# Performance work log

Measured on AMD Instinct MI355X. Metric: run time of the kernel, lower is better.

Reference implementation:

```python
import jax, jax.numpy as jnp
import numpy as np

POS_THRESHOLD = 0.5
B, N, A = 8, 262144, 64


def setup_inputs() -> dict:
    key = jax.random.key(0)
    k1, k2, k3 = jax.random.split(key, 3)
    # anchors: (y_center, x_center, h, w); centers in [0,1), positive h,w
    anchorss = jax.random.uniform(k1, (B, N, 4), dtype=jnp.float32)
    anchorss = anchorss.at[..., 2:].set(anchorss[..., 2:] * 0.3 + 0.01)  # h,w in (0.01, 0.31)
    # gt boxes as (y1, x1, y2, x2) with y1<y2, x1<x2
    raw = jax.random.uniform(k2, (B, A, 2, 2), dtype=jnp.float32)  # [...,coord_pair,(lo,hi)]
    lo = jnp.min(raw, axis=-1)  # (B,A,2) -> y1,x1
    hi = jnp.max(raw, axis=-1)  # (B,A,2) -> y2,x2
    gt_bboxess = jnp.concatenate([lo, hi], axis=-1)  # (B,A,4) = (y1,x1,y2,x2)
    gt_counts = jax.random.randint(k3, (B, 1), 1, A, dtype=jnp.int32)
    return {"anchorss": anchorss, "gt_bboxess": gt_bboxess,
            "gt_counts": gt_counts, "use_anchor": 1}


def reference(anchorss, gt_bboxess, gt_counts, use_anchor):
    # anchorss: (B,N,4), gt_bboxess: (B,A,4), gt_counts: (B,1)
    if use_anchor:
        y, x, h, w = (anchorss[..., i] for i in range(4))  # (B,N)
        y1 = y - h / 2
        y2 = y1 + h
        x1 = x - w / 2
        x2 = x1 + w
        area = h * w
    else:
        y1, x1, y2, x2 = (anchorss[..., i] for i in range(4))
        area = (y2 - y1) * (x2 - x1)
    gy1, gx1, gy2, gx2 = (gt_bboxess[..., i] for i in range(4))  # (B,A)
    ga = (gy2 - gy1) * (gx2 - gx1)  # (B,A)
    # broadcast anchors (B,N,1) against gts (B,1,A): same clamp math as torch
    yy1 = jnp.clip(y1[:, :, None], gy1[:, None, :], gy2[:, None, :])
    xx1 = jnp.clip(x1[:, :, None], gx1[:, None, :], gx2[:, None, :])
    yy2 = jnp.clip(y2[:, :, None], gy1[:, None, :], gy2[:, None, :])
    xx2 = jnp.clip(x2[:, :, None], gx1[:, None, :], gx2[:, None, :])
    inter = (yy2 - yy1) * (xx2 - xx1)  # (B,N,A)
    union = area[:, :, None] + ga[:, None, :] - inter
    iou = inter / union
    # mask out invalid gts (index >= gt_count per batch)
    valid = jnp.arange(A, dtype=gt_counts.dtype)[None, :] < gt_counts  # (B,A)
    pos = (iou >= POS_THRESHOLD) & valid[:, None, :]  # (B,N,A)
    labels = jnp.any(pos, axis=2).astype(jnp.int32)[..., None]  # (B,N,1)
    return labels
```

## Files before the change

kernel.cpp:

```cpp
#include <hip/hip_runtime.h>

constexpr int BLOCK = 256;
constexpr int IPT = 4;

__global__ __launch_bounds__(BLOCK) void assign_cls_label_kernel(
    const float* __restrict__ anchorss,
    const float* __restrict__ gt_bboxess,
    const int* __restrict__ gt_counts,
    const int* __restrict__ use_anchor_p,
    int* __restrict__ out,
    int N, int A)
{
#pragma clang fp contract(off)
    extern __shared__ float smem[];
    float4* s_box = reinterpret_cast<float4*>(smem);
    float*  s_ga  = smem + 4 * A;
    __shared__ int s_count;

    const int b   = blockIdx.y;
    const int tid = threadIdx.x;

    for (int i = tid; i < A; i += BLOCK) {
        float4 g = reinterpret_cast<const float4*>(gt_bboxess)[(size_t)b * A + i];
        s_box[i] = g;
        s_ga[i]  = (g.z - g.x) * (g.w - g.y);
    }
    if (tid == 0) s_count = gt_counts[b];
    __syncthreads();

    const int count      = s_count;
    const int use_anchor = use_anchor_p[0];

    const int n0 = (blockIdx.x * BLOCK + tid) * IPT;
    if (n0 >= N) return;
    const int nk = min(IPT, N - n0);

    float y1[IPT], x1[IPT], y2[IPT], x2[IPT], area[IPT];
    const float4* arow = reinterpret_cast<const float4*>(anchorss) + (size_t)b * N;
    for (int k = 0; k < IPT; ++k) {
        const int n = (k < nk) ? (n0 + k) : (N - 1);
        float4 a = arow[n];
        if (use_anchor) {
            const float h = a.z, w = a.w;
            y1[k]   = a.x - h * 0.5f;
            y2[k]   = y1[k] + h;
            x1[k]   = a.y - w * 0.5f;
            x2[k]   = x1[k] + w;
            area[k] = h * w;
        } else {
            y1[k] = a.x; x1[k] = a.y; y2[k] = a.z; x2[k] = a.w;
            area[k] = (y2[k] - y1[k]) * (x2[k] - x1[k]);
        }
    }

    int pos[IPT] = {0, 0, 0, 0};
    for (int gi = 0; gi < count; ++gi) {
        const float4 g  = s_box[gi];
        const float  ga = s_ga[gi];
#pragma unroll
        for (int k = 0; k < IPT; ++k) {
            const float yy1 = __builtin_amdgcn_fmed3f(y1[k], g.x, g.z);
            const float yy2 = __builtin_amdgcn_fmed3f(y2[k], g.x, g.z);
            const float xx1 = __builtin_amdgcn_fmed3f(x1[k], g.y, g.w);
            const float xx2 = __builtin_amdgcn_fmed3f(x2[k], g.y, g.w);
            const float inter = (yy2 - yy1) * (xx2 - xx1);
            const float u     = (area[k] + ga) - inter;
            const float hu    = 0.5f * u;
            pos[k] |= (inter >= hu);
            if (__builtin_expect((inter < hu) & (inter >= hu * 0.99999988f), 0)) {
                pos[k] |= ((inter / u) >= 0.5f);
            }
        }
    }

    const size_t ob = (size_t)b * N + n0;
    if (nk == IPT) {
        *reinterpret_cast<int4*>(out + ob) = make_int4(pos[0], pos[1], pos[2], pos[3]);
    } else {
        for (int k = 0; k < nk; ++k) out[ob + k] = pos[k];
    }
}

extern "C" void kernel_launch(void* const* d_in, const int* in_sizes, int n_in,
                              void* d_out, int out_size, void* d_ws, size_t ws_size,
                              hipStream_t stream) {
    const float* anchorss   = (const float*)d_in[0];
    const float* gt_bboxess = (const float*)d_in[1];
    const int*   gt_counts  = (const int*)d_in[2];
    const int*   use_anchor = (const int*)d_in[3];
    int*         out        = (int*)d_out;

    const int B = in_sizes[2];
    const int A = in_sizes[1] / (4 * B);
    const int N = in_sizes[0] / (4 * B);

    dim3 grid((N + BLOCK * IPT - 1) / (BLOCK * IPT), B);
    size_t smem = (size_t)(5 * A) * sizeof(float);
    hipLaunchKernelGGL(assign_cls_label_kernel, grid, dim3(BLOCK), smem, stream,
                       anchorss, gt_bboxess, gt_counts, use_anchor, out, N, A);
}
```

Before: 109.3 us.

## Process two batches per block, front-load loads, replace IoU branch with fma margin

```diff
diff --git a/kernel.cpp b/kernel.cpp
--- a/kernel.cpp
+++ b/kernel.cpp
@@ -2,82 +2,98 @@
 
 constexpr int BLOCK = 256;
 constexpr int IPT = 4;
+constexpr int BPB = 2;
 
-__global__ __launch_bounds__(BLOCK) void assign_cls_label_kernel(
+__global__ __launch_bounds__(BLOCK, 4) void assign_cls_label_kernel(
     const float* __restrict__ anchorss,
     const float* __restrict__ gt_bboxess,
     const int* __restrict__ gt_counts,
     const int* __restrict__ use_anchor_p,
     int* __restrict__ out,
-    int N, int A)
+    int N, int A, int B)
 {
 #pragma clang fp contract(off)
-    extern __shared__ float smem[];
-    float4* s_box = reinterpret_cast<float4*>(smem);
-    float*  s_ga  = smem + 4 * A;
-    __shared__ int s_count;
+    extern __shared__ float4 s_box[];
+    __shared__ int s_count[BPB];
 
-    const int b   = blockIdx.y;
     const int tid = threadIdx.x;
+    const int b0  = blockIdx.y * BPB;
+    const int nb  = (B - b0 < BPB) ? (B - b0) : BPB;
 
-    for (int i = tid; i < A; i += BLOCK) {
-        float4 g = reinterpret_cast<const float4*>(gt_bboxess)[(size_t)b * A + i];
-        s_box[i] = g;
-        s_ga[i]  = (g.z - g.x) * (g.w - g.y);
+    for (int i = tid; i < nb * A; i += BLOCK) {
+        const int bb = i / A, gi = i - bb * A;
+        s_box[i] = reinterpret_cast<const float4*>(gt_bboxess)[(size_t)(b0 + bb) * A + gi];
     }
-    if (tid == 0) s_count = gt_counts[b];
+    if (tid < nb) s_count[tid] = gt_counts[b0 + tid];
+
+    const int use_anchor = use_anchor_p[0];
+    const int base_n = blockIdx.x * (BLOCK * IPT) + tid;
+
+    float4 a[BPB][IPT];
+#pragma unroll
+    for (int bb = 0; bb < BPB; ++bb)
+#pragma unroll
+        for (int k = 0; k < IPT; ++k) {
+            int n = base_n + k * BLOCK;
+            if (n >= N) n = N - 1;
+            if (bb < nb)
+                a[bb][k] = reinterpret_cast<const float4*>(anchorss)[(size_t)(b0 + bb) * N + n];
+        }
+
     __syncthreads();
 
-    const int count      = s_count;
-    const int use_anchor = use_anchor_p[0];
+    const float c26 = 1.0f / 67108864.0f;
 
-    const int n0 = (blockIdx.x * BLOCK + tid) * IPT;
-    if (n0 >= N) return;
-    const int nk = min(IPT, N - n0);
-
-    float y1[IPT], x1[IPT], y2[IPT], x2[IPT], area[IPT];
-    const float4* arow = reinterpret_cast<const float4*>(anchorss) + (size_t)b * N;
-    for (int k = 0; k < IPT; ++k) {
-        const int n = (k < nk) ? (n0 + k) : (N - 1);
-        float4 a = arow[n];
-        if (use_anchor) {
-            const float h = a.z, w = a.w;
-            y1[k]   = a.x - h * 0.5f;
-            y2[k]   = y1[k] + h;
-            x1[k]   = a.y - w * 0.5f;
-            x2[k]   = x1[k] + w;
-            area[k] = h * w;
-        } else {
-            y1[k] = a.x; x1[k] = a.y; y2[k] = a.z; x2[k] = a.w;
-            area[k] = (y2[k] - y1[k]) * (x2[k] - x1[k]);
-        }
-    }
-
-    int pos[IPT] = {0, 0, 0, 0};
-    for (int gi = 0; gi < count; ++gi) {
-        const float4 g  = s_box[gi];
-        const float  ga = s_ga[gi];
+    for (int bb = 0; bb < nb; ++bb) {
+        float y1[IPT], x1[IPT], y2[IPT], x2[IPT], area[IPT], acc[IPT];
 #pragma unroll
         for (int k = 0; k < IPT; ++k) {
-            const float yy1 = __builtin_amdgcn_fmed3f(y1[k], g.x, g.z);
-            const float yy2 = __builtin_amdgcn_fmed3f(y2[k], g.x, g.z);
-            const float xx1 = __builtin_amdgcn_fmed3f(x1[k], g.y, g.w);
-            const float xx2 = __builtin_amdgcn_fmed3f(x2[k], g.y, g.w);
-            const float inter = (yy2 - yy1) * (xx2 - xx1);
-            const float u     = (area[k] + ga) - inter;
-            const float hu    = 0.5f * u;
-            pos[k] |= (inter >= hu);
-            if (__builtin_expect((inter < hu) & (inter >= hu * 0.99999988f), 0)) {
-                pos[k] |= ((inter / u) >= 0.5f);
+            const float4 v = a[bb][k];
+            if (use_anchor) {
+                const float h = v.z, w = v.w;
+                y1[k]   = v.x - h * 0.5f;
+                y2[k]   = y1[k] + h;
+                x1[k]   = v.y - w * 0.5f;
+                x2[k]   = x1[k] + w;
+                area[k] = h * w;
+            } else {
+                y1[k] = v.x; x1[k] = v.y; y2[k] = v.z; x2[k] = v.w;
+                area[k] = (y2[k] - y1[k]) * (x2[k] - x1[k]);
             }
+            acc[k] = -1.0f;
         }
-    }
 
-    const size_t ob = (size_t)b * N + n0;
-    if (nk == IPT) {
-        *reinterpret_cast<int4*>(out + ob) = make_int4(pos[0], pos[1], pos[2], pos[3]);
-    } else {
-        for (int k = 0; k < nk; ++k) out[ob + k] = pos[k];
+        const int count = s_count[bb];
+        const float4* sb = s_box + bb * A;
+
+        float4 g = sb[0];
+        for (int gi = 0; gi < count; ++gi) {
+            int ni = gi + 1; if (ni >= A) ni = A - 1;
+            const float4 gn = sb[ni];
+            const float ga = (g.z - g.x) * (g.w - g.y);
+#pragma unroll
+            for (int k = 0; k < IPT; ++k) {
+                const float yy1 = __builtin_amdgcn_fmed3f(y1[k], g.x, g.z);
+                const float yy2 = __builtin_amdgcn_fmed3f(y2[k], g.x, g.z);
+                const float xx1 = __builtin_amdgcn_fmed3f(x1[k], g.y, g.w);
+                const float xx2 = __builtin_amdgcn_fmed3f(x2[k], g.y, g.w);
+                const float dy    = yy2 - yy1;
+                const float dx    = xx2 - xx1;
+                const float inter = dy * dx;
+                const float s     = area[k] + ga;
+                const float u     = s - inter;
+                const float e = fmaf(-0.5f, u, inter);
+                const float r = fmaf(c26, u, e);
+                acc[k] = fmaxf(acc[k], r);
+            }
+            g = gn;
+        }
+
+#pragma unroll
+        for (int k = 0; k < IPT; ++k) {
+            const int n = base_n + k * BLOCK;
+            if (n < N) out[(size_t)(b0 + bb) * N + n] = (acc[k] >= 0.0f) ? 1 : 0;
+        }
     }
 }
 
@@ -94,8 +110,8 @@
     const int A = in_sizes[1] / (4 * B);
     const int N = in_sizes[0] / (4 * B);
 
-    dim3 grid((N + BLOCK * IPT - 1) / (BLOCK * IPT), B);
-    size_t smem = (size_t)(5 * A) * sizeof(float);
+    dim3 grid((N + BLOCK * IPT - 1) / (BLOCK * IPT), (B + BPB - 1) / BPB);
+    size_t smem = (size_t)(BPB * A) * sizeof(float4);
     hipLaunchKernelGGL(assign_cls_label_kernel, grid, dim3(BLOCK), smem, stream,
-                       anchorss, gt_bboxess, gt_counts, use_anchor, out, N, A);
+                       anchorss, gt_bboxess, gt_counts, use_anchor, out, N, A, B);
 }
```

Result: no change. 110.8 us (+1.4%).

## Process all batches per block with packed f32x2 math and branchless threshold test

Applied to the files above, without the earlier changes.

```diff
diff --git a/kernel.cpp b/kernel.cpp
--- a/kernel.cpp
+++ b/kernel.cpp
@@ -1,83 +1,134 @@
 #include <hip/hip_runtime.h>
 
+typedef float f32x2 __attribute__((ext_vector_type(2)));
+
 constexpr int BLOCK = 256;
-constexpr int IPT = 4;
+constexpr int IPT   = 2;
+constexpr int BPB   = 8;
 
-__global__ __launch_bounds__(BLOCK) void assign_cls_label_kernel(
+__global__ __launch_bounds__(BLOCK, 2) void assign_cls_label_kernel(
     const float* __restrict__ anchorss,
     const float* __restrict__ gt_bboxess,
     const int* __restrict__ gt_counts,
     const int* __restrict__ use_anchor_p,
     int* __restrict__ out,
-    int N, int A)
+    int N, int A, int B)
 {
 #pragma clang fp contract(off)
     extern __shared__ float smem[];
-    float4* s_box = reinterpret_cast<float4*>(smem);
-    float*  s_ga  = smem + 4 * A;
-    __shared__ int s_count;
+    float4* s_box = (float4*)smem;
+    float*  s_ga  = smem + 4 * BPB * A;
+    __shared__ int s_count[BPB];
 
-    const int b   = blockIdx.y;
     const int tid = threadIdx.x;
+    const int b0  = blockIdx.y * BPB;
+    const int nbA = ((B - b0 < BPB) ? (B - b0) : BPB) * A;
 
-    for (int i = tid; i < A; i += BLOCK) {
-        float4 g = reinterpret_cast<const float4*>(gt_bboxess)[(size_t)b * A + i];
+    const int n0r = blockIdx.x * (BLOCK * IPT) + tid;
+    const int n1r = n0r + BLOCK;
+    const int n0  = (n0r < N) ? n0r : N - 1;
+    const int n1  = (n1r < N) ? n1r : N - 1;
+
+    float4 an0 = ((const float4*)anchorss)[(size_t)b0 * N + n0];
+    float4 an1 = ((const float4*)anchorss)[(size_t)b0 * N + n1];
+
+    for (int i = tid; i < nbA; i += BLOCK) {
+        const int bb = i / A, gi = i - bb * A;
+        float4 g = ((const float4*)gt_bboxess)[(size_t)(b0 + bb) * A + gi];
         s_box[i] = g;
         s_ga[i]  = (g.z - g.x) * (g.w - g.y);
     }
-    if (tid == 0) s_count = gt_counts[b];
+    if (tid < BPB) s_count[tid] = (b0 + tid < B) ? gt_counts[b0 + tid] : 0;
+
+    const int use_anchor = use_anchor_p[0];
     __syncthreads();
 
-    const int count      = s_count;
-    const int use_anchor = use_anchor_p[0];
+    const float c26 = 1.0f / 67108864.0f;
+    const int   Am1 = A - 1;
 
-    const int n0 = (blockIdx.x * BLOCK + tid) * IPT;
-    if (n0 >= N) return;
-    const int nk = min(IPT, N - n0);
+    for (int bb = 0; bb < BPB; ++bb) {
+        if (b0 + bb >= B) break;
+        const float4 ac0 = an0, ac1 = an1;
+        if (bb + 1 < BPB && b0 + bb + 1 < B) {
+            const float4* arow = (const float4*)anchorss + (size_t)(b0 + bb + 1) * N;
+            an0 = arow[n0];
+            an1 = arow[n1];
+        }
 
-    float y1[IPT], x1[IPT], y2[IPT], x2[IPT], area[IPT];
-    const float4* arow = reinterpret_cast<const float4*>(anchorss) + (size_t)b * N;
-    for (int k = 0; k < IPT; ++k) {
-        const int n = (k < nk) ? (n0 + k) : (N - 1);
-        float4 a = arow[n];
+        f32x2 Y1, X1, Y2, X2, AREA;
         if (use_anchor) {
-            const float h = a.z, w = a.w;
-            y1[k]   = a.x - h * 0.5f;
-            y2[k]   = y1[k] + h;
-            x1[k]   = a.y - w * 0.5f;
-            x2[k]   = x1[k] + w;
-            area[k] = h * w;
+            Y1.x = ac0.x - ac0.z * 0.5f;  Y1.y = ac1.x - ac1.z * 0.5f;
+            Y2.x = Y1.x + ac0.z;          Y2.y = Y1.y + ac1.z;
+            X1.x = ac0.y - ac0.w * 0.5f;  X1.y = ac1.y - ac1.w * 0.5f;
+            X2.x = X1.x + ac0.w;          X2.y = X1.y + ac1.w;
+            AREA.x = ac0.z * ac0.w;       AREA.y = ac1.z * ac1.w;
         } else {
-            y1[k] = a.x; x1[k] = a.y; y2[k] = a.z; x2[k] = a.w;
-            area[k] = (y2[k] - y1[k]) * (x2[k] - x1[k]);
+            Y1.x = ac0.x; Y1.y = ac1.x;   X1.x = ac0.y; X1.y = ac1.y;
+            Y2.x = ac0.z; Y2.y = ac1.z;   X2.x = ac0.w; X2.y = ac1.w;
+            AREA.x = (Y2.x - Y1.x) * (X2.x - X1.x);
+            AREA.y = (Y2.y - Y1.y) * (X2.y - X1.y);
         }
-    }
+        f32x2 ACC; ACC.x = -1.0f; ACC.y = -1.0f;
 
-    int pos[IPT] = {0, 0, 0, 0};
-    for (int gi = 0; gi < count; ++gi) {
-        const float4 g  = s_box[gi];
-        const float  ga = s_ga[gi];
-#pragma unroll
-        for (int k = 0; k < IPT; ++k) {
-            const float yy1 = __builtin_amdgcn_fmed3f(y1[k], g.x, g.z);
-            const float yy2 = __builtin_amdgcn_fmed3f(y2[k], g.x, g.z);
-            const float xx1 = __builtin_amdgcn_fmed3f(x1[k], g.y, g.w);
-            const float xx2 = __builtin_amdgcn_fmed3f(x2[k], g.y, g.w);
-            const float inter = (yy2 - yy1) * (xx2 - xx1);
-            const float u     = (area[k] + ga) - inter;
-            const float hu    = 0.5f * u;
-            pos[k] |= (inter >= hu);
-            if (__builtin_expect((inter < hu) & (inter >= hu * 0.99999988f), 0)) {
-                pos[k] |= ((inter / u) >= 0.5f);
-            }
+        const float4* sb    = s_box + bb * A;
+        const float*  sga   = s_ga  + bb * A;
+        const int     count = s_count[bb];
+
+        auto comp = [&](const float4 g, const float ga) {
+            f32x2 yy1, yy2, xx1, xx2;
+            yy1.x = __builtin_amdgcn_fmed3f(Y1.x, g.x, g.z);
+            yy1.y = __builtin_amdgcn_fmed3f(Y1.y, g.x, g.z);
+            yy2.x = __builtin_amdgcn_fmed3f(Y2.x, g.x, g.z);
+            yy2.y = __builtin_amdgcn_fmed3f(Y2.y, g.x, g.z);
+            xx1.x = __builtin_amdgcn_fmed3f(X1.x, g.y, g.w);
+            xx1.y = __builtin_amdgcn_fmed3f(X1.y, g.y, g.w);
+            xx2.x = __builtin_amdgcn_fmed3f(X2.x, g.y, g.w);
+            xx2.y = __builtin_amdgcn_fmed3f(X2.y, g.y, g.w);
+            f32x2 dy    = yy2 - yy1;
+            f32x2 dx    = xx2 - xx1;
+            f32x2 inter = dy * dx;
+            f32x2 u     = (AREA + ga) - inter;
+            f32x2 hn; hn.x = -0.5f; hn.y = -0.5f;
+            f32x2 cc; cc.x = c26;   cc.y = c26;
+            f32x2 e = __builtin_elementwise_fma(u, hn, inter);
+            f32x2 r = __builtin_elementwise_fma(u, cc, e);
+            ACC = __builtin_elementwise_max(ACC, r);
+        };
+
+        float4 gA0, gA1, gA2, gA3, gB0, gB1, gB2, gB3;
+        float  aA0, aA1, aA2, aA3, aB0, aB1, aB2, aB3;
+
+#define LOAD_BANK(G0,G1,G2,G3,Q0,Q1,Q2,Q3, base_) do {                       \
+            int i0_ = (base_),   i1_ = (base_)+1, i2_ = (base_)+2, i3_ = (base_)+3; \
+            i0_ = (i0_ < Am1) ? i0_ : Am1;  i1_ = (i1_ < Am1) ? i1_ : Am1;   \
+            i2_ = (i2_ < Am1) ? i2_ : Am1;  i3_ = (i3_ < Am1) ? i3_ : Am1;   \
+            G0 = sb[i0_]; Q0 = sga[i0_];  G1 = sb[i1_]; Q1 = sga[i1_];       \
+            G2 = sb[i2_]; Q2 = sga[i2_];  G3 = sb[i3_]; Q3 = sga[i3_];       \
+        } while (0)
+
+        LOAD_BANK(gA0,gA1,gA2,gA3, aA0,aA1,aA2,aA3, 0);
+        int gi = 0;
+        while (gi + 8 <= count) {
+            LOAD_BANK(gB0,gB1,gB2,gB3, aB0,aB1,aB2,aB3, gi + 4);
+            comp(gA0,aA0); comp(gA1,aA1); comp(gA2,aA2); comp(gA3,aA3);
+            LOAD_BANK(gA0,gA1,gA2,gA3, aA0,aA1,aA2,aA3, gi + 8);
+            comp(gB0,aB0); comp(gB1,aB1); comp(gB2,aB2); comp(gB3,aB3);
+            gi += 8;
         }
-    }
+        const int rem = count - gi;
+        if (rem > 4) LOAD_BANK(gB0,gB1,gB2,gB3, aB0,aB1,aB2,aB3, gi + 4);
+        if (rem > 0) comp(gA0, aA0);
+        if (rem > 1) comp(gA1, aA1);
+        if (rem > 2) comp(gA2, aA2);
+        if (rem > 3) comp(gA3, aA3);
+        if (rem > 4) comp(gB0, aB0);
+        if (rem > 5) comp(gB1, aB1);
+        if (rem > 6) comp(gB2, aB2);
+#undef LOAD_BANK
 
-    const size_t ob = (size_t)b * N + n0;
-    if (nk == IPT) {
-        *reinterpret_cast<int4*>(out + ob) = make_int4(pos[0], pos[1], pos[2], pos[3]);
-    } else {
-        for (int k = 0; k < nk; ++k) out[ob + k] = pos[k];
+        int* orow = out + (size_t)(b0 + bb) * N;
+        if (n0r < N) orow[n0r] = (ACC.x >= 0.0f) ? 1 : 0;
+        if (n1r < N) orow[n1r] = (ACC.y >= 0.0f) ? 1 : 0;
     }
 }
 
@@ -94,8 +145,8 @@
     const int A = in_sizes[1] / (4 * B);
     const int N = in_sizes[0] / (4 * B);
 
-    dim3 grid((N + BLOCK * IPT - 1) / (BLOCK * IPT), B);
-    size_t smem = (size_t)(5 * A) * sizeof(float);
+    dim3 grid((N + BLOCK * IPT - 1) / (BLOCK * IPT), (B + BPB - 1) / BPB);
+    size_t smem = (size_t)(BPB * A) * (sizeof(float4) + sizeof(float));
     hipLaunchKernelGGL(assign_cls_label_kernel, grid, dim3(BLOCK), smem, stream,
-                       anchorss, gt_bboxess, gt_counts, use_anchor, out, N, A);
+                       anchorss, gt_bboxess, gt_counts, use_anchor, out, N, A, B);
 }
```

Result: faster. 98.85 us (-9.5%).
